# Kernel optimization log

Hardware: AMD Instinct MI355X
Metric: run time of the kernel (lower is better)

Reference implementation:

```python
import jax, jax.numpy as jnp
import numpy as np

EMPHASIS_FACTOR = 1.5
TOP_K_PERCENT = 0.2


def setup_inputs() -> dict:
    key = jax.random.key(0)
    k1, k2 = jax.random.split(key)
    B, S, D = 32, 8192, 256
    x = jax.random.normal(k1, (B, S, D), dtype=jnp.float32)
    W = jax.random.normal(k2, (D, 1), dtype=jnp.float32) * (1.0 / np.sqrt(D))
    b = jnp.zeros((1,), dtype=jnp.float32)
    return {"x": x, "W": W, "b": b}


def reference(x, W, b):
    B, S, D = x.shape
    # e = tanh(x @ W + b): [B, S, 1]
    e = jnp.tanh(jnp.einsum('bsd,do->bso', x, W) + b)
    # softmax over seq axis, squeeze -> [B, S]
    a = jax.nn.softmax(e, axis=1)[..., 0]
    # top-k selection: k = max(1, int(S * top_k_percent)), static under jit
    k = max(1, int(S * TOP_K_PERCENT))
    _, top_k_idx = jax.lax.top_k(a, k)  # [B, k]
    # mask of top-k positions (equiv to one_hot + reduce_max, but a direct scatter)
    mask = jnp.zeros((B, S), dtype=bool).at[jnp.arange(B)[:, None], top_k_idx].set(True)
    emphasized_a = jnp.where(mask, a * EMPHASIS_FACTOR, a)  # [B, S]
    # weighted sum over seq -> [B, D]
    summed_output = jnp.einsum('bsd,bs->bd', x, emphasized_a)
    return summed_output, emphasized_a
```

## Files before the change

### kernel.cpp

```cpp
#include <hip/hip_runtime.h>
#include <math.h>

#define BB 32
#define SS 8192
#define DD 256
#define K_SEL 1638
#define EMPH 1.5f
#define NCHUNK 64
#define ROWS_PER_BLOCK (SS / NCHUNK)

__global__ __launch_bounds__(256) void k1_dot_tanh(const float* __restrict__ x,
                                                   const float* __restrict__ W,
                                                   const float* __restrict__ bias,
                                                   float* __restrict__ e) {
    const int lane = threadIdx.x & 63;
    const int wib  = threadIdx.x >> 6;
    const int wavesPerBlock = blockDim.x >> 6;
    const int waveId = blockIdx.x * wavesPerBlock + wib;
    const int totalWaves = gridDim.x * wavesPerBlock;
    const float4 w4 = ((const float4*)W)[lane];
    const float bias0 = bias[0];
    const int totalRows = BB * SS;
    for (int row = waveId; row < totalRows; row += totalWaves) {
        float4 x4 = ((const float4*)(x + (size_t)row * DD))[lane];
        float p = x4.x * w4.x + x4.y * w4.y + x4.z * w4.z + x4.w * w4.w;
        #pragma unroll
        for (int off = 32; off >= 1; off >>= 1)
            p += __shfl_xor(p, off, 64);
        if (lane == 0) e[row] = tanhf(p + bias0);
    }
}

__global__ __launch_bounds__(1024) void k2_softmax_topk(float* __restrict__ ea) {
    const int b = blockIdx.x;
    const int tid = threadIdx.x;
    const int lane = tid & 63;
    const int wid  = tid >> 6;

    __shared__ float se[SS];
    __shared__ float wredf[16];
    __shared__ unsigned hist[256];
    __shared__ unsigned ssum[256];
    __shared__ unsigned wcnt[16];
    __shared__ unsigned uvar[3];
    __shared__ float fvar[2];

    float* eg = ea + (size_t)b * SS;

    float lmax = -3.0e38f;
    #pragma unroll
    for (int i = 0; i < 8; i++) {
        int s = tid + i * 1024;
        float v = eg[s];
        se[s] = v;
        lmax = fmaxf(lmax, v);
    }
    #pragma unroll
    for (int off = 32; off >= 1; off >>= 1)
        lmax = fmaxf(lmax, __shfl_xor(lmax, off, 64));
    if (lane == 0) wredf[wid] = lmax;
    __syncthreads();
    if (tid == 0) {
        float m = wredf[0];
        for (int w = 1; w < 16; w++) m = fmaxf(m, wredf[w]);
        fvar[0] = m;
    }
    __syncthreads();
    const float m = fvar[0];

    float lsum = 0.0f;
    #pragma unroll
    for (int i = 0; i < 8; i++) {
        int s = tid + i * 1024;
        lsum += expf(se[s] - m);
    }
    #pragma unroll
    for (int off = 32; off >= 1; off >>= 1)
        lsum += __shfl_xor(lsum, off, 64);
    if (lane == 0) wredf[wid] = lsum;
    __syncthreads();
    if (tid == 0) {
        float z = 0.0f;
        for (int w = 0; w < 16; w++) z += wredf[w];
        fvar[1] = 1.0f / z;
    }
    __syncthreads();
    const float invZ = fvar[1];

    unsigned kk = K_SEL;
    unsigned prefix = 0;
    for (int byte = 3; byte >= 0; byte--) {
        if (tid < 256) hist[tid] = 0;
        __syncthreads();
        #pragma unroll
        for (int i = 0; i < 8; i++) {
            int s = tid + i * 1024;
            unsigned u = __float_as_uint(se[s]);
            unsigned key = u ^ ((u & 0x80000000u) ? 0xFFFFFFFFu : 0x80000000u);
            bool active = (byte == 3) || ((key >> ((byte + 1) * 8)) == prefix);
            if (active) atomicAdd(&hist[(key >> (byte * 8)) & 0xFFu], 1u);
        }
        __syncthreads();
        if (tid < 256) ssum[tid] = hist[tid];
        __syncthreads();
        for (int off = 1; off < 256; off <<= 1) {
            unsigned add = 0;
            if (tid < 256 && tid + off < 256) add = ssum[tid + off];
            __syncthreads();
            if (tid < 256) ssum[tid] += add;
            __syncthreads();
        }
        if (tid < 256) {
            unsigned above = (tid == 255) ? 0u : ssum[tid + 1];
            if (above < kk && kk <= ssum[tid]) {
                uvar[0] = (unsigned)tid;
                uvar[1] = kk - above;
            }
        }
        __syncthreads();
        prefix = (prefix << 8) | uvar[0];
        kk = uvar[1];
        __syncthreads();
    }
    const unsigned T = prefix;
    const unsigned r = kk;

    if (tid == 0) uvar[2] = 0;
    __syncthreads();
    for (int chunk = 0; chunk < 8; chunk++) {
        int s = chunk * 1024 + tid;
        float v = se[s];
        unsigned u = __float_as_uint(v);
        unsigned key = u ^ ((u & 0x80000000u) ? 0xFFFFFFFFu : 0x80000000u);
        bool gt = key > T;
        bool eq = (key == T);
        unsigned long long bal = __ballot(eq);
        unsigned waveTot = (unsigned)__popcll(bal);
        unsigned myPref = (unsigned)__popcll(bal & ((1ull << lane) - 1ull));
        if (lane == 0) wcnt[wid] = waveTot;
        __syncthreads();
        unsigned base = uvar[2];
        for (int w = 0; w < wid; w++) base += wcnt[w];
        unsigned rank = base + myPref;
        bool sel = gt || (eq && rank < r);
        float a = expf(v - m) * invZ;
        eg[s] = sel ? a * EMPH : a;
        __syncthreads();
        if (tid == 0) {
            unsigned t = uvar[2];
            for (int w = 0; w < 16; w++) t += wcnt[w];
            uvar[2] = t;
        }
        __syncthreads();
    }
}

__global__ __launch_bounds__(256) void k3_weighted_partial(const float* __restrict__ x,
                                                           const float* __restrict__ ea,
                                                           float* __restrict__ part) {
    const int blk = blockIdx.x;
    const int b = blk / NCHUNK;
    const int chunk = blk % NCHUNK;
    const int lane = threadIdx.x & 63;
    const int wid  = threadIdx.x >> 6;
    const float* xb = x + ((size_t)b * SS + (size_t)chunk * ROWS_PER_BLOCK) * DD;
    const float* ab = ea + (size_t)b * SS + (size_t)chunk * ROWS_PER_BLOCK;
    float4 acc = make_float4(0.f, 0.f, 0.f, 0.f);
    for (int rr = wid; rr < ROWS_PER_BLOCK; rr += 4) {
        float4 x4 = ((const float4*)(xb + (size_t)rr * DD))[lane];
        float a = ab[rr];
        acc.x += x4.x * a; acc.y += x4.y * a; acc.z += x4.z * a; acc.w += x4.w * a;
    }
    __shared__ float lds[4 * 256];
    ((float4*)lds)[wid * 64 + lane] = acc;
    __syncthreads();
    const int t = threadIdx.x;
    float v = lds[0 * 256 + t] + lds[1 * 256 + t] + lds[2 * 256 + t] + lds[3 * 256 + t];
    part[(size_t)blk * 256 + t] = v;
}

__global__ __launch_bounds__(256) void k0_zero(float* __restrict__ p, int n) {
    int i = blockIdx.x * blockDim.x + threadIdx.x;
    if (i < n) p[i] = 0.0f;
}
__global__ __launch_bounds__(256) void k3_weighted_atomic(const float* __restrict__ x,
                                                          const float* __restrict__ ea,
                                                          float* __restrict__ out) {
    const int blk = blockIdx.x;
    const int b = blk / NCHUNK;
    const int chunk = blk % NCHUNK;
    const int lane = threadIdx.x & 63;
    const int wid  = threadIdx.x >> 6;
    const float* xb = x + ((size_t)b * SS + (size_t)chunk * ROWS_PER_BLOCK) * DD;
    const float* ab = ea + (size_t)b * SS + (size_t)chunk * ROWS_PER_BLOCK;
    float4 acc = make_float4(0.f, 0.f, 0.f, 0.f);
    for (int rr = wid; rr < ROWS_PER_BLOCK; rr += 4) {
        float4 x4 = ((const float4*)(xb + (size_t)rr * DD))[lane];
        float a = ab[rr];
        acc.x += x4.x * a; acc.y += x4.y * a; acc.z += x4.z * a; acc.w += x4.w * a;
    }
    __shared__ float lds[4 * 256];
    ((float4*)lds)[wid * 64 + lane] = acc;
    __syncthreads();
    const int t = threadIdx.x;
    float v = lds[0 * 256 + t] + lds[1 * 256 + t] + lds[2 * 256 + t] + lds[3 * 256 + t];
    atomicAdd(&out[b * 256 + t], v);
}

__global__ __launch_bounds__(256) void k4_reduce(const float* __restrict__ part,
                                                 float* __restrict__ out) {
    const int b = blockIdx.x;
    const int d = threadIdx.x;
    float s = 0.0f;
    for (int c = 0; c < NCHUNK; c++)
        s += part[((size_t)b * NCHUNK + c) * 256 + d];
    out[b * 256 + d] = s;
}

extern "C" void kernel_launch(void* const* d_in, const int* in_sizes, int n_in,
                              void* d_out, int out_size, void* d_ws, size_t ws_size,
                              hipStream_t stream) {
    const float* x    = (const float*)d_in[0];
    const float* W    = (const float*)d_in[1];
    const float* bias = (const float*)d_in[2];
    float* out = (float*)d_out;
    float* sum_out = out;
    float* ea = out + BB * DD;

    k1_dot_tanh<<<4096, 256, 0, stream>>>(x, W, bias, ea);
    k2_softmax_topk<<<BB, 1024, 0, stream>>>(ea);

    const size_t part_bytes = (size_t)BB * NCHUNK * 256 * sizeof(float);
    if (ws_size >= part_bytes) {
        float* part = (float*)d_ws;
        k3_weighted_partial<<<BB * NCHUNK, 256, 0, stream>>>(x, ea, part);
        k4_reduce<<<BB, 256, 0, stream>>>(part, sum_out);
    } else {
        k0_zero<<<(BB * DD + 255) / 256, 256, 0, stream>>>(sum_out, BB * DD);
        k3_weighted_atomic<<<BB * NCHUNK, 256, 0, stream>>>(x, ea, sum_out);
    }
}
```

Before: 415.9 us.

## Fuse coarse top-k histogram into score kernel and drop softmax max pass

The score kernel now processes four rows per wave, with 16 lanes per row, and builds a 2048-bin histogram of the tanh scores in shared memory. Per-chunk histograms go to workspace. The select kernel merges them to find the top-11-bit prefix, then refines with three 7-bit passes instead of four 8-bit radix passes. The softmax max reduction is removed because tanh output lies in [-1,1], so exp cannot overflow. This path requires a larger workspace; otherwise it falls back to the old kernels.

```diff
diff --git a/kernel.cpp b/kernel.cpp
--- a/kernel.cpp
+++ b/kernel.cpp
@@ -8,130 +8,191 @@
 #define EMPH 1.5f
 #define NCHUNK 64
 #define ROWS_PER_BLOCK (SS / NCHUNK)
-
-__global__ __launch_bounds__(256) void k1_dot_tanh(const float* __restrict__ x,
-                                                   const float* __restrict__ W,
-                                                   const float* __restrict__ bias,
-                                                   float* __restrict__ e) {
-    const int lane = threadIdx.x & 63;
-    const int wib  = threadIdx.x >> 6;
-    const int wavesPerBlock = blockDim.x >> 6;
-    const int waveId = blockIdx.x * wavesPerBlock + wib;
-    const int totalWaves = gridDim.x * wavesPerBlock;
-    const float4 w4 = ((const float4*)W)[lane];
+#define HBINS 2048
+#define HCH 8
+
+__device__ __forceinline__ unsigned monokey(float f) {
+    unsigned u = __float_as_uint(f);
+    return u ^ ((u & 0x80000000u) ? 0xFFFFFFFFu : 0x80000000u);
+}
+
+__global__ __launch_bounds__(1024) void k1_e_hist(const float* __restrict__ x,
+                                                  const float* __restrict__ W,
+                                                  const float* __restrict__ bias,
+                                                  float* __restrict__ e_ws,
+                                                  unsigned* __restrict__ hist_ws) {
+    __shared__ unsigned hist[HBINS];
+    const int tid = threadIdx.x;
+    const int lane = tid & 63;
+    const int wv = tid >> 6;
+    for (int i = tid; i < HBINS; i += 1024) hist[i] = 0;
+
+    const int b = blockIdx.x >> 3;
+    const int ch = blockIdx.x & 7;
+    const int row0 = ch * 1024;
+
+    const float4* W4 = (const float4*)W;
+    const int cg = lane & 15;
+    const float4 w0 = W4[cg];
+    const float4 w1 = W4[cg + 16];
+    const float4 w2 = W4[cg + 32];
+    const float4 w3 = W4[cg + 48];
     const float bias0 = bias[0];
-    const int totalRows = BB * SS;
-    for (int row = waveId; row < totalRows; row += totalWaves) {
-        float4 x4 = ((const float4*)(x + (size_t)row * DD))[lane];
-        float p = x4.x * w4.x + x4.y * w4.y + x4.z * w4.z + x4.w * w4.w;
-        #pragma unroll
-        for (int off = 32; off >= 1; off >>= 1)
-            p += __shfl_xor(p, off, 64);
-        if (lane == 0) e[row] = tanhf(p + bias0);
-    }
-}
-
-__global__ __launch_bounds__(1024) void k2_softmax_topk(float* __restrict__ ea) {
+    __syncthreads();
+
+    const float* xb = x + (size_t)b * SS * DD;
+    float* eb = e_ws + (size_t)b * SS;
+
+    for (int it = 0; it < 16; it++) {
+        const int r = row0 + (it * 16 + wv) * 4 + (lane >> 4);
+        const float4* rp = (const float4*)(xb + (size_t)r * DD);
+        float4 a0 = rp[cg];
+        float4 a1 = rp[cg + 16];
+        float4 a2 = rp[cg + 32];
+        float4 a3 = rp[cg + 48];
+        float p = a0.x * w0.x + a0.y * w0.y + a0.z * w0.z + a0.w * w0.w;
+        p += a1.x * w1.x + a1.y * w1.y + a1.z * w1.z + a1.w * w1.w;
+        p += a2.x * w2.x + a2.y * w2.y + a2.z * w2.z + a2.w * w2.w;
+        p += a3.x * w3.x + a3.y * w3.y + a3.z * w3.z + a3.w * w3.w;
+        p += __shfl_xor(p, 1, 64);
+        p += __shfl_xor(p, 2, 64);
+        p += __shfl_xor(p, 4, 64);
+        p += __shfl_xor(p, 8, 64);
+        if (cg == 0) {
+            float e = tanhf(p + bias0);
+            eb[r] = e;
+            atomicAdd(&hist[monokey(e) >> 21], 1u);
+        }
+    }
+    __syncthreads();
+    unsigned* hout = hist_ws + (size_t)blockIdx.x * HBINS;
+    for (int i = tid; i < HBINS; i += 1024) hout[i] = hist[i];
+}
+
+__global__ __launch_bounds__(1024) void k2_select(const float* __restrict__ e_ws,
+                                                  const unsigned* __restrict__ hist_ws,
+                                                  float* __restrict__ ea_out) {
     const int b = blockIdx.x;
     const int tid = threadIdx.x;
     const int lane = tid & 63;
-    const int wid  = tid >> 6;
+    const int wid = tid >> 6;
 
     __shared__ float se[SS];
     __shared__ float wredf[16];
-    __shared__ unsigned hist[256];
-    __shared__ unsigned ssum[256];
+    __shared__ unsigned binTot[HBINS];
+    __shared__ unsigned gsuf[256];
+    __shared__ unsigned h7[128];
     __shared__ unsigned wcnt[16];
     __shared__ unsigned uvar[3];
-    __shared__ float fvar[2];
-
-    float* eg = ea + (size_t)b * SS;
-
-    float lmax = -3.0e38f;
+    __shared__ float fvar[1];
+
+    const float* eg = e_ws + (size_t)b * SS;
+    float* og = ea_out + (size_t)b * SS;
+
+    float lsum = 0.0f;
     #pragma unroll
     for (int i = 0; i < 8; i++) {
         int s = tid + i * 1024;
         float v = eg[s];
         se[s] = v;
-        lmax = fmaxf(lmax, v);
-    }
-    #pragma unroll
-    for (int off = 32; off >= 1; off >>= 1)
-        lmax = fmaxf(lmax, __shfl_xor(lmax, off, 64));
-    if (lane == 0) wredf[wid] = lmax;
-    __syncthreads();
-    if (tid == 0) {
-        float m = wredf[0];
-        for (int w = 1; w < 16; w++) m = fmaxf(m, wredf[w]);
-        fvar[0] = m;
-    }
-    __syncthreads();
-    const float m = fvar[0];
-
-    float lsum = 0.0f;
-    #pragma unroll
-    for (int i = 0; i < 8; i++) {
-        int s = tid + i * 1024;
-        lsum += expf(se[s] - m);
+        lsum += expf(v);
     }
     #pragma unroll
     for (int off = 32; off >= 1; off >>= 1)
         lsum += __shfl_xor(lsum, off, 64);
     if (lane == 0) wredf[wid] = lsum;
-    __syncthreads();
+
+    unsigned c0 = 0, c1 = 0;
+    for (int ch = 0; ch < HCH; ch++) {
+        const unsigned* hc = hist_ws + ((size_t)(b * HCH + ch)) * HBINS;
+        c0 += hc[2 * tid];
+        c1 += hc[2 * tid + 1];
+    }
+    binTot[2 * tid] = c0;
+    binTot[2 * tid + 1] = c1;
+    __syncthreads();
+
     if (tid == 0) {
         float z = 0.0f;
         for (int w = 0; w < 16; w++) z += wredf[w];
-        fvar[1] = 1.0f / z;
-    }
-    __syncthreads();
-    const float invZ = fvar[1];
-
-    unsigned kk = K_SEL;
-    unsigned prefix = 0;
-    for (int byte = 3; byte >= 0; byte--) {
-        if (tid < 256) hist[tid] = 0;
+        fvar[0] = 1.0f / z;
+    }
+    if (tid < 256) {
+        unsigned g = 0;
+        #pragma unroll
+        for (int j = 0; j < 8; j++) g += binTot[tid * 8 + j];
+        gsuf[tid] = g;
+    }
+    __syncthreads();
+    for (int off = 1; off < 256; off <<= 1) {
+        unsigned add = 0;
+        if (tid < 256 && tid + off < 256) add = gsuf[tid + off];
+        __syncthreads();
+        if (tid < 256) gsuf[tid] += add;
+        __syncthreads();
+    }
+    if (tid < 256) {
+        unsigned above = (tid == 255) ? 0u : gsuf[tid + 1];
+        if (above < K_SEL && K_SEL <= gsuf[tid]) {
+            unsigned running = above;
+            for (int j = 7; j >= 0; j--) {
+                int bin = tid * 8 + j;
+                unsigned c = binTot[bin];
+                if (running < K_SEL && K_SEL <= running + c) {
+                    uvar[0] = (unsigned)bin;
+                    uvar[1] = K_SEL - running;
+                    break;
+                }
+                running += c;
+            }
+        }
+    }
+    __syncthreads();
+    unsigned prefix = uvar[0];
+    unsigned kk = uvar[1];
+
+    #pragma unroll
+    for (int pass = 0; pass < 3; pass++) {
+        const int shift = 14 - 7 * pass;
+        if (tid < 128) h7[tid] = 0;
         __syncthreads();
         #pragma unroll
         for (int i = 0; i < 8; i++) {
             int s = tid + i * 1024;
-            unsigned u = __float_as_uint(se[s]);
-            unsigned key = u ^ ((u & 0x80000000u) ? 0xFFFFFFFFu : 0x80000000u);
-            bool active = (byte == 3) || ((key >> ((byte + 1) * 8)) == prefix);
-            if (active) atomicAdd(&hist[(key >> (byte * 8)) & 0xFFu], 1u);
-        }
-        __syncthreads();
-        if (tid < 256) ssum[tid] = hist[tid];
-        __syncthreads();
-        for (int off = 1; off < 256; off <<= 1) {
+            unsigned key = monokey(se[s]);
+            if ((key >> (shift + 7)) == prefix)
+                atomicAdd(&h7[(key >> shift) & 127u], 1u);
+        }
+        __syncthreads();
+        for (int off = 1; off < 128; off <<= 1) {
             unsigned add = 0;
-            if (tid < 256 && tid + off < 256) add = ssum[tid + off];
+            if (tid < 128 && tid + off < 128) add = h7[tid + off];
             __syncthreads();
-            if (tid < 256) ssum[tid] += add;
+            if (tid < 128) h7[tid] += add;
             __syncthreads();
         }
-        if (tid < 256) {
-            unsigned above = (tid == 255) ? 0u : ssum[tid + 1];
-            if (above < kk && kk <= ssum[tid]) {
-                uvar[0] = (unsigned)tid;
+        if (tid < 128) {
+            unsigned above = (tid == 127) ? 0u : h7[tid + 1];
+            if (above < kk && kk <= h7[tid]) {
+                uvar[0] = (prefix << 7) | (unsigned)tid;
                 uvar[1] = kk - above;
             }
         }
         __syncthreads();
-        prefix = (prefix << 8) | uvar[0];
+        prefix = uvar[0];
         kk = uvar[1];
         __syncthreads();
     }
     const unsigned T = prefix;
     const unsigned r = kk;
+    const float invZ = fvar[0];
 
     if (tid == 0) uvar[2] = 0;
     __syncthreads();
     for (int chunk = 0; chunk < 8; chunk++) {
         int s = chunk * 1024 + tid;
         float v = se[s];
-        unsigned u = __float_as_uint(v);
-        unsigned key = u ^ ((u & 0x80000000u) ? 0xFFFFFFFFu : 0x80000000u);
+        unsigned key = monokey(v);
         bool gt = key > T;
         bool eq = (key == T);
         unsigned long long bal = __ballot(eq);
@@ -143,8 +204,8 @@
         for (int w = 0; w < wid; w++) base += wcnt[w];
         unsigned rank = base + myPref;
         bool sel = gt || (eq && rank < r);
-        float a = expf(v - m) * invZ;
-        eg[s] = sel ? a * EMPH : a;
+        float a = expf(v) * invZ;
+        og[s] = sel ? a * EMPH : a;
         __syncthreads();
         if (tid == 0) {
             unsigned t = uvar[2];
@@ -179,11 +240,135 @@
     part[(size_t)blk * 256 + t] = v;
 }
 
-__global__ __launch_bounds__(256) void k0_zero(float* __restrict__ p, int n) {
+__global__ __launch_bounds__(256) void k4_reduce(const float* __restrict__ part,
+                                                 float* __restrict__ out) {
+    const int b = blockIdx.x;
+    const int d = threadIdx.x;
+    float s = 0.0f;
+    for (int c = 0; c < NCHUNK; c++)
+        s += part[((size_t)b * NCHUNK + c) * 256 + d];
+    out[b * 256 + d] = s;
+}
+
+__global__ __launch_bounds__(256) void f1_dot_tanh(const float* __restrict__ x,
+                                                   const float* __restrict__ W,
+                                                   const float* __restrict__ bias,
+                                                   float* __restrict__ e) {
+    const int lane = threadIdx.x & 63;
+    const int wib  = threadIdx.x >> 6;
+    const int waveId = blockIdx.x * 4 + wib;
+    const int totalWaves = gridDim.x * 4;
+    const float4 w4 = ((const float4*)W)[lane];
+    const float bias0 = bias[0];
+    for (int row = waveId; row < BB * SS; row += totalWaves) {
+        float4 x4 = ((const float4*)(x + (size_t)row * DD))[lane];
+        float p = x4.x * w4.x + x4.y * w4.y + x4.z * w4.z + x4.w * w4.w;
+        #pragma unroll
+        for (int off = 32; off >= 1; off >>= 1)
+            p += __shfl_xor(p, off, 64);
+        if (lane == 0) e[row] = tanhf(p + bias0);
+    }
+}
+__global__ __launch_bounds__(1024) void f2_softmax_topk(float* __restrict__ ea) {
+    const int b = blockIdx.x;
+    const int tid = threadIdx.x;
+    const int lane = tid & 63;
+    const int wid  = tid >> 6;
+    __shared__ float se[SS];
+    __shared__ float wredf[16];
+    __shared__ unsigned hist[256];
+    __shared__ unsigned ssum[256];
+    __shared__ unsigned wcnt[16];
+    __shared__ unsigned uvar[3];
+    __shared__ float fvar[1];
+    float* eg = ea + (size_t)b * SS;
+    float lsum = 0.0f;
+    #pragma unroll
+    for (int i = 0; i < 8; i++) {
+        int s = tid + i * 1024;
+        float v = eg[s];
+        se[s] = v;
+        lsum += expf(v);
+    }
+    #pragma unroll
+    for (int off = 32; off >= 1; off >>= 1)
+        lsum += __shfl_xor(lsum, off, 64);
+    if (lane == 0) wredf[wid] = lsum;
+    __syncthreads();
+    if (tid == 0) {
+        float z = 0.0f;
+        for (int w = 0; w < 16; w++) z += wredf[w];
+        fvar[0] = 1.0f / z;
+    }
+    __syncthreads();
+    const float invZ = fvar[0];
+    unsigned kk = K_SEL;
+    unsigned prefix = 0;
+    for (int byte = 3; byte >= 0; byte--) {
+        if (tid < 256) hist[tid] = 0;
+        __syncthreads();
+        #pragma unroll
+        for (int i = 0; i < 8; i++) {
+            unsigned key = monokey(se[tid + i * 1024]);
+            bool active = (byte == 3) || ((key >> ((byte + 1) * 8)) == prefix);
+            if (active) atomicAdd(&hist[(key >> (byte * 8)) & 0xFFu], 1u);
+        }
+        __syncthreads();
+        if (tid < 256) ssum[tid] = hist[tid];
+        __syncthreads();
+        for (int off = 1; off < 256; off <<= 1) {
+            unsigned add = 0;
+            if (tid < 256 && tid + off < 256) add = ssum[tid + off];
+            __syncthreads();
+            if (tid < 256) ssum[tid] += add;
+            __syncthreads();
+        }
+        if (tid < 256) {
+            unsigned above = (tid == 255) ? 0u : ssum[tid + 1];
+            if (above < kk && kk <= ssum[tid]) {
+                uvar[0] = (unsigned)tid;
+                uvar[1] = kk - above;
+            }
+        }
+        __syncthreads();
+        prefix = (prefix << 8) | uvar[0];
+        kk = uvar[1];
+        __syncthreads();
+    }
+    const unsigned T = prefix;
+    const unsigned r = kk;
+    if (tid == 0) uvar[2] = 0;
+    __syncthreads();
+    for (int chunk = 0; chunk < 8; chunk++) {
+        int s = chunk * 1024 + tid;
+        float v = se[s];
+        unsigned key = monokey(v);
+        bool gt = key > T;
+        bool eq = (key == T);
+        unsigned long long bal = __ballot(eq);
+        unsigned waveTot = (unsigned)__popcll(bal);
+        unsigned myPref = (unsigned)__popcll(bal & ((1ull << lane) - 1ull));
+        if (lane == 0) wcnt[wid] = waveTot;
+        __syncthreads();
+        unsigned base = uvar[2];
+        for (int w = 0; w < wid; w++) base += wcnt[w];
+        bool sel = gt || (eq && (base + myPref) < r);
+        float a = expf(v) * invZ;
+        eg[s] = sel ? a * EMPH : a;
+        __syncthreads();
+        if (tid == 0) {
+            unsigned t = uvar[2];
+            for (int w = 0; w < 16; w++) t += wcnt[w];
+            uvar[2] = t;
+        }
+        __syncthreads();
+    }
+}
+__global__ __launch_bounds__(256) void f0_zero(float* __restrict__ p, int n) {
     int i = blockIdx.x * blockDim.x + threadIdx.x;
     if (i < n) p[i] = 0.0f;
 }
-__global__ __launch_bounds__(256) void k3_weighted_atomic(const float* __restrict__ x,
+__global__ __launch_bounds__(256) void f3_weighted_atomic(const float* __restrict__ x,
                                                           const float* __restrict__ ea,
                                                           float* __restrict__ out) {
     const int blk = blockIdx.x;
@@ -207,19 +392,10 @@
     atomicAdd(&out[b * 256 + t], v);
 }
 
-__global__ __launch_bounds__(256) void k4_reduce(const float* __restrict__ part,
-                                                 float* __restrict__ out) {
-    const int b = blockIdx.x;
-    const int d = threadIdx.x;
-    float s = 0.0f;
-    for (int c = 0; c < NCHUNK; c++)
-        s += part[((size_t)b * NCHUNK + c) * 256 + d];
-    out[b * 256 + d] = s;
-}
-
 extern "C" void kernel_launch(void* const* d_in, const int* in_sizes, int n_in,
                               void* d_out, int out_size, void* d_ws, size_t ws_size,
                               hipStream_t stream) {
+    (void)in_sizes; (void)n_in; (void)out_size;
     const float* x    = (const float*)d_in[0];
     const float* W    = (const float*)d_in[1];
     const float* bias = (const float*)d_in[2];
@@ -227,16 +403,27 @@
     float* sum_out = out;
     float* ea = out + BB * DD;
 
-    k1_dot_tanh<<<4096, 256, 0, stream>>>(x, W, bias, ea);
-    k2_softmax_topk<<<BB, 1024, 0, stream>>>(ea);
-
+    const size_t e_bytes    = (size_t)BB * SS * sizeof(float);
+    const size_t hist_bytes = (size_t)BB * HCH * HBINS * sizeof(unsigned);
     const size_t part_bytes = (size_t)BB * NCHUNK * 256 * sizeof(float);
-    if (ws_size >= part_bytes) {
-        float* part = (float*)d_ws;
+    if (ws_size >= e_bytes + hist_bytes + part_bytes) {
+        float* e_ws       = (float*)d_ws;
+        unsigned* hist_ws = (unsigned*)((char*)d_ws + e_bytes);
+        float* part       = (float*)((char*)d_ws + e_bytes + hist_bytes);
+        k1_e_hist<<<BB * HCH, 1024, 0, stream>>>(x, W, bias, e_ws, hist_ws);
+        k2_select<<<BB, 1024, 0, stream>>>(e_ws, hist_ws, ea);
         k3_weighted_partial<<<BB * NCHUNK, 256, 0, stream>>>(x, ea, part);
         k4_reduce<<<BB, 256, 0, stream>>>(part, sum_out);
     } else {
-        k0_zero<<<(BB * DD + 255) / 256, 256, 0, stream>>>(sum_out, BB * DD);
-        k3_weighted_atomic<<<BB * NCHUNK, 256, 0, stream>>>(x, ea, sum_out);
-    }
-}
+        f1_dot_tanh<<<4096, 256, 0, stream>>>(x, W, bias, ea);
+        f2_softmax_topk<<<BB, 1024, 0, stream>>>(ea);
+        if (ws_size >= part_bytes) {
+            float* part = (float*)d_ws;
+            k3_weighted_partial<<<BB * NCHUNK, 256, 0, stream>>>(x, ea, part);
+            k4_reduce<<<BB, 256, 0, stream>>>(part, sum_out);
+        } else {
+            f0_zero<<<(BB * DD + 255) / 256, 256, 0, stream>>>(sum_out, BB * DD);
+            f3_weighted_atomic<<<BB * NCHUNK, 256, 0, stream>>>(x, ea, sum_out);
+        }
+    }
+}
```

Measured after the change: 417.5 us. No clear change (+0.4%).
